# Kernel optimization log

Measured on AMD Instinct MI355X. Metric: run time of the kernel, lower is better.

The kernel has to match this reference:

```python
import jax, jax.numpy as jnp
import numpy as np

EMBED_DIM = 512
NUM_HEADS = 8
HEAD_DIM = EMBED_DIM // NUM_HEADS


def setup_inputs() -> dict:
    key = jax.random.key(0)
    ks = jax.random.split(key, 5)
    B, N, D = 2, 4096, EMBED_DIM
    s_in = 1.0 / np.sqrt(D)
    x = jax.random.normal(ks[0], (B, N, D), dtype=jnp.float32)
    qkv_w = jax.random.uniform(ks[1], (3 * D, D), dtype=jnp.float32, minval=-s_in, maxval=s_in)
    qkv_b = jax.random.uniform(ks[2], (3 * D,), dtype=jnp.float32, minval=-s_in, maxval=s_in)
    out_w = jax.random.uniform(ks[3], (D, D), dtype=jnp.float32, minval=-s_in, maxval=s_in)
    out_b = jax.random.uniform(ks[4], (D,), dtype=jnp.float32, minval=-s_in, maxval=s_in)
    return {"x": x, "qkv_w": qkv_w, "qkv_b": qkv_b, "out_w": out_w, "out_b": out_b}


def reference(x, qkv_w, qkv_b, out_w, out_b):
    B, N, D = x.shape
    H, Hd = NUM_HEADS, HEAD_DIM
    # qkv projection: [B,N,3D] -> [3,B,H,N,Hd]
    qkv = x @ qkv_w.T + qkv_b
    qkv = qkv.reshape(B, N, 3, H, Hd).transpose(2, 0, 3, 1, 4)
    q, k, v = qkv[0], qkv[1], qkv[2]
    scale = 1.0 / jnp.sqrt(jnp.asarray(Hd, dtype=x.dtype))
    scores = jnp.einsum("bhnd,bhmd->bhnm", q, k) * scale  # [B,H,N,N]
    weights = jax.nn.softmax(scores, axis=-1)
    out = jnp.einsum("bhnm,bhmd->bhnd", weights, v)  # [B,H,N,Hd]
    out = out.transpose(0, 2, 1, 3).reshape(B, N, D)
    return out @ out_w.T + out_b
```

## Files before the change

kernel.cpp:

```cpp
#include <hip/hip_runtime.h>

typedef __attribute__((ext_vector_type(8))) short short8;
typedef __attribute__((ext_vector_type(2))) float f32x2;
typedef __attribute__((ext_vector_type(4))) float f32x4;
typedef __attribute__((ext_vector_type(16))) float f32x16;
typedef unsigned short u16;
typedef unsigned int u32;

#define SCQ 0.18033688011112042f

__device__ __forceinline__ u16 f2b(float f) {
  unsigned u = __builtin_bit_cast(unsigned, f);
  u += 0x7FFFu + ((u >> 16) & 1u);
  return (u16)(u >> 16);
}

__device__ __forceinline__ u32 cvtpk(float a, float b) {
  u32 r;
  asm("v_cvt_pk_bf16_f32 %0, %1, %2" : "=v"(r) : "v"(a), "v"(b));
  return r;
}

__device__ __forceinline__ float ex2(float x) { return __builtin_amdgcn_exp2f(x); }

__global__ __launch_bounds__(256) void convert_k(
    const float* __restrict__ x, const float* __restrict__ w1, const float* __restrict__ w2,
    u16* __restrict__ xb, u16* __restrict__ w1b, u16* __restrict__ w2b) {
  const int NXv = (8192 * 512) / 4;
  const int NW1v = (1536 * 512) / 4;
  const int NW2v = (512 * 512) / 4;
  int i = blockIdx.x * 256 + threadIdx.x;
  const float4* src;
  u16* dst;
  int j;
  float scale = 1.0f;
  if (i < NXv) {
    src = (const float4*)x; dst = xb; j = i;
  } else if (i < NXv + NW1v) {
    j = i - NXv; src = (const float4*)w1; dst = w1b;
    if (j < (512 * 512) / 4) scale = SCQ;
  } else {
    j = i - NXv - NW1v;
    if (j >= NW2v) return;
    src = (const float4*)w2; dst = w2b;
  }
  float4 v = src[j];
  ushort4 o;
  o.x = f2b(v.x * scale); o.y = f2b(v.y * scale);
  o.z = f2b(v.z * scale); o.w = f2b(v.w * scale);
  *reinterpret_cast<ushort4*>(dst + (size_t)j * 4) = o;
}

__global__ __launch_bounds__(256) void qkv_gemm(
    const u16* __restrict__ Ab, const u16* __restrict__ Bw, const float* __restrict__ bias,
    u16* __restrict__ Qd, u16* __restrict__ Kd, u16* __restrict__ Vtd) {
  const int m0 = blockIdx.x * 128, n0 = blockIdx.y * 64;
  const int tid = threadIdx.x, wave = tid >> 6, lane = tid & 63;
  const int g = lane >> 4, lr = lane & 15;
  const int wm = (wave >> 1) * 64, wn = (wave & 1) * 32;
  __shared__ alignas(16) u16 Al[128][72];
  __shared__ alignas(16) u16 Bl[64][72];

  f32x4 acc[4][2];
#pragma unroll
  for (int mf = 0; mf < 4; ++mf)
#pragma unroll
    for (int nf = 0; nf < 2; ++nf)
#pragma unroll
      for (int r = 0; r < 4; ++r) acc[mf][nf][r] = 0.0f;

  const int rr = tid >> 3, cc = tid & 7;
  for (int k0 = 0; k0 < 512; k0 += 64) {
    __syncthreads();
#pragma unroll
    for (int it = 0; it < 4; ++it)
      *reinterpret_cast<short8*>(&Al[rr + it * 32][cc * 8]) =
          *reinterpret_cast<const short8*>(Ab + (size_t)(m0 + rr + it * 32) * 512 + k0 + cc * 8);
#pragma unroll
    for (int it = 0; it < 2; ++it)
      *reinterpret_cast<short8*>(&Bl[rr + it * 32][cc * 8]) =
          *reinterpret_cast<const short8*>(Bw + (size_t)(n0 + rr + it * 32) * 512 + k0 + cc * 8);
    __syncthreads();
#pragma unroll
    for (int kb = 0; kb < 2; ++kb) {
      short8 bf[2], af[4];
#pragma unroll
      for (int nf = 0; nf < 2; ++nf)
        bf[nf] = *reinterpret_cast<const short8*>(&Bl[wn + nf * 16 + lr][kb * 32 + g * 8]);
#pragma unroll
      for (int mf = 0; mf < 4; ++mf)
        af[mf] = *reinterpret_cast<const short8*>(&Al[wm + mf * 16 + lr][kb * 32 + g * 8]);
#pragma unroll
      for (int mf = 0; mf < 4; ++mf)
#pragma unroll
        for (int nf = 0; nf < 2; ++nf)
          acc[mf][nf] = __builtin_amdgcn_mfma_f32_16x16x32_bf16(af[mf], bf[nf], acc[mf][nf], 0, 0, 0);
    }
  }
#pragma unroll
  for (int mf = 0; mf < 4; ++mf)
#pragma unroll
    for (int nf = 0; nf < 2; ++nf)
#pragma unroll
      for (int r = 0; r < 4; ++r) {
        int row = m0 + wm + mf * 16 + g * 4 + r;
        int col = n0 + wn + nf * 16 + lr;
        float bv = bias[col];
        if (col < 512) bv *= SCQ;
        u16 val = f2b(acc[mf][nf][r] + bv);
        int which = col >> 9, dcol = col & 511;
        int h = dcol >> 6, hd = dcol & 63;
        int b = row >> 12, n = row & 4095;
        size_t hb = (size_t)(b * 8 + h);
        if (which == 0)      Qd[(hb * 4096 + n) * 64 + hd] = val;
        else if (which == 1) Kd[(hb * 4096 + n) * 64 + hd] = val;
        else                 Vtd[(hb * 64 + hd) * 4096 + n] = val;
      }
}

__global__ __launch_bounds__(256, 2) void attn10(
    const u16* __restrict__ Qd, const u16* __restrict__ Kd, const u16* __restrict__ Vtd,
    float* __restrict__ Op, float* __restrict__ Lp) {
  int f = blockIdx.x;
  int xcd = f & 7, slot = f >> 3;
  int bh = (xcd << 1) + (slot >> 6);
  int rem = slot & 63;
  int quarter = rem >> 4;
  int qb = rem & 15;

  const int tid = threadIdx.x, wave = tid >> 6, lane = tid & 63;
  const int hi = lane >> 5, lq = lane & 31;

  const u16* Qh = Qd + (size_t)bh * (4096 * 64);
  const u16* Kh = Kd + (size_t)bh * (4096 * 64);
  const u16* Vh = Vtd + (size_t)bh * (64 * 4096);
  float* Oh = Op + (size_t)quarter * (8192 * 512);
  float* Lh = Lp + (size_t)quarter * (16 * 4096);

  __shared__ alignas(16) u16 Kl[2][64 * 64];

  const int qrow_base = qb * 256 + wave * 64;

  short8 qf[2][4];
#pragma unroll
  for (int qt = 0; qt < 2; ++qt)
#pragma unroll
    for (int s = 0; s < 4; ++s)
      qf[qt][s] = *reinterpret_cast<const short8*>(
          Qh + (size_t)(qrow_base + qt * 32 + lq) * 64 + s * 16 + hi * 8);

  f32x16 acc[2][2];
#pragma unroll
  for (int qt = 0; qt < 2; ++qt)
#pragma unroll
    for (int dt = 0; dt < 2; ++dt)
#pragma unroll
      for (int i = 0; i < 16; ++i) acc[qt][dt][i] = 0.0f;

  f32x16 Z;
#pragma unroll
  for (int i = 0; i < 16; ++i) Z[i] = 0.0f;

  float lrun[2] = {0.0f, 0.0f};

  const int kv0 = quarter * 1024;
  const int g0 = tid, g1 = tid + 256;
  const int sr0 = g0 >> 3, sc0 = g0 & 7;
  const int sr1 = g1 >> 3, sc1 = g1 & 7;

  {
    short8 t0 = *reinterpret_cast<const short8*>(Kh + (size_t)(kv0 + sr0) * 64 + sc0 * 8);
    short8 t1 = *reinterpret_cast<const short8*>(Kh + (size_t)(kv0 + sr1) * 64 + sc1 * 8);
    *reinterpret_cast<short8*>(&Kl[0][sr0 * 64 + ((sc0 ^ (sr0 & 7)) << 3)]) = t0;
    *reinterpret_cast<short8*>(&Kl[0][sr1 * 64 + ((sc1 ^ (sr1 & 7)) << 3)]) = t1;
  }
  __syncthreads();

#pragma unroll 1
  for (int kt = 0; kt < 16; ++kt) {
    const int cur = kt & 1;
    const int kbase = kv0 + kt * 64;
    short8 t0, t1;
    const bool pf = (kt + 1 < 16);
    if (pf) {
      t0 = *reinterpret_cast<const short8*>(Kh + (size_t)(kbase + 64 + sr0) * 64 + sc0 * 8);
      t1 = *reinterpret_cast<const short8*>(Kh + (size_t)(kbase + 64 + sr1) * 64 + sc1 * 8);
    }

    f32x16 st[2][2];
#pragma unroll
    for (int s = 0; s < 4; ++s) {
      const int ch = ((2 * s + hi) ^ (lq & 7)) << 3;
      short8 kf0 = *reinterpret_cast<const short8*>(&Kl[cur][lq * 64 + ch]);
      short8 kf1 = *reinterpret_cast<const short8*>(&Kl[cur][(32 + lq) * 64 + ch]);
      if (s == 0) {
        st[0][0] = __builtin_amdgcn_mfma_f32_32x32x16_bf16(kf0, qf[0][0], Z, 0, 0, 0);
        st[0][1] = __builtin_amdgcn_mfma_f32_32x32x16_bf16(kf1, qf[0][0], Z, 0, 0, 0);
        st[1][0] = __builtin_amdgcn_mfma_f32_32x32x16_bf16(kf0, qf[1][0], Z, 0, 0, 0);
        st[1][1] = __builtin_amdgcn_mfma_f32_32x32x16_bf16(kf1, qf[1][0], Z, 0, 0, 0);
      } else {
        st[0][0] = __builtin_amdgcn_mfma_f32_32x32x16_bf16(kf0, qf[0][s], st[0][0], 0, 0, 0);
        st[0][1] = __builtin_amdgcn_mfma_f32_32x32x16_bf16(kf1, qf[0][s], st[0][1], 0, 0, 0);
        st[1][0] = __builtin_amdgcn_mfma_f32_32x32x16_bf16(kf0, qf[1][s], st[1][0], 0, 0, 0);
        st[1][1] = __builtin_amdgcn_mfma_f32_32x32x16_bf16(kf1, qf[1][s], st[1][1], 0, 0, 0);
      }
    }

    short8 vf[4][2];
#pragma unroll
    for (int ks = 0; ks < 4; ++ks)
#pragma unroll
      for (int dt = 0; dt < 2; ++dt)
        vf[ks][dt] = *reinterpret_cast<const short8*>(
            Vh + (size_t)(dt * 32 + lq) * 4096 + kbase + ks * 16 + hi * 8);

    short8 pb[2][4];
#pragma unroll
    for (int qt = 0; qt < 2; ++qt) {
      f32x2 p2[16];
#pragma unroll
      for (int j = 0; j < 8; ++j) {
        p2[j][0] = ex2(st[qt][0][2 * j]);
        p2[j][1] = ex2(st[qt][0][2 * j + 1]);
        p2[8 + j][0] = ex2(st[qt][1][2 * j]);
        p2[8 + j][1] = ex2(st[qt][1][2 * j + 1]);
      }
      f32x2 s0 = (p2[0] + p2[1]) + (p2[2] + p2[3]);
      f32x2 s1 = (p2[4] + p2[5]) + (p2[6] + p2[7]);
      f32x2 s2 = (p2[8] + p2[9]) + (p2[10] + p2[11]);
      f32x2 s3 = (p2[12] + p2[13]) + (p2[14] + p2[15]);
      f32x2 sm = (s0 + s1) + (s2 + s3);
      lrun[qt] += sm[0] + sm[1];
#pragma unroll
      for (int ks = 0; ks < 4; ++ks) {
        u32 wa = cvtpk(p2[4 * ks + 0][0], p2[4 * ks + 0][1]);
        u32 wb = cvtpk(p2[4 * ks + 2][0], p2[4 * ks + 2][1]);
        u32 wc = cvtpk(p2[4 * ks + 1][0], p2[4 * ks + 1][1]);
        u32 wd = cvtpk(p2[4 * ks + 3][0], p2[4 * ks + 3][1]);
        asm volatile("v_permlane32_swap_b32 %0, %1" : "+v"(wa), "+v"(wb));
        asm volatile("v_permlane32_swap_b32 %0, %1" : "+v"(wc), "+v"(wd));
        int4 wv;
        wv.x = (int)wa; wv.y = (int)wc; wv.z = (int)wb; wv.w = (int)wd;
        pb[qt][ks] = __builtin_bit_cast(short8, wv);
      }
    }

#pragma unroll
    for (int ks = 0; ks < 4; ++ks) {
      acc[0][0] = __builtin_amdgcn_mfma_f32_32x32x16_bf16(vf[ks][0], pb[0][ks], acc[0][0], 0, 0, 0);
      acc[0][1] = __builtin_amdgcn_mfma_f32_32x32x16_bf16(vf[ks][1], pb[0][ks], acc[0][1], 0, 0, 0);
      acc[1][0] = __builtin_amdgcn_mfma_f32_32x32x16_bf16(vf[ks][0], pb[1][ks], acc[1][0], 0, 0, 0);
      acc[1][1] = __builtin_amdgcn_mfma_f32_32x32x16_bf16(vf[ks][1], pb[1][ks], acc[1][1], 0, 0, 0);
    }

    if (pf) {
      *reinterpret_cast<short8*>(&Kl[cur ^ 1][sr0 * 64 + ((sc0 ^ (sr0 & 7)) << 3)]) = t0;
      *reinterpret_cast<short8*>(&Kl[cur ^ 1][sr1 * 64 + ((sc1 ^ (sr1 & 7)) << 3)]) = t1;
    }
    __syncthreads();
  }

  const int b = bh >> 3, h = bh & 7;
#pragma unroll
  for (int qt = 0; qt < 2; ++qt) {
    const int qn = qrow_base + qt * 32 + lq;
    const size_t rowoff = ((size_t)(b * 4096 + qn)) * 512 + h * 64;
#pragma unroll
    for (int dt = 0; dt < 2; ++dt)
#pragma unroll
      for (int t = 0; t < 4; ++t) {
        f32x4 v4;
        v4[0] = acc[qt][dt][4 * t + 0];
        v4[1] = acc[qt][dt][4 * t + 1];
        v4[2] = acc[qt][dt][4 * t + 2];
        v4[3] = acc[qt][dt][4 * t + 3];
        *reinterpret_cast<f32x4*>(Oh + rowoff + dt * 32 + t * 8 + hi * 4) = v4;
      }
    float lt = lrun[qt] + __shfl_xor(lrun[qt], 32);
    if (hi == 0) Lh[(bh << 12) + qn] = lt;
  }
}

__global__ __launch_bounds__(256) void combine_k(
    const float* __restrict__ Op, const float* __restrict__ Lp,
    u16* __restrict__ attnb) {
  int idx = blockIdx.x * 256 + threadIdx.x;
  int row = idx >> 7, c4 = idx & 127;
  int b = row >> 12, n = row & 4095, h = c4 >> 4;
  int li = (((b << 3) + h) << 12) + n;
  float l = (Lp[li] + Lp[li + 65536]) + (Lp[li + 131072] + Lp[li + 196608]);
  float inv = 1.0f / l;
  const int STRIDE = 8192 * 512 / 4;
  float4 o0 = reinterpret_cast<const float4*>(Op)[idx];
  float4 o1 = reinterpret_cast<const float4*>(Op)[idx + STRIDE];
  float4 o2 = reinterpret_cast<const float4*>(Op)[idx + 2 * STRIDE];
  float4 o3 = reinterpret_cast<const float4*>(Op)[idx + 3 * STRIDE];
  ushort4 o;
  o.x = f2b(((o0.x + o1.x) + (o2.x + o3.x)) * inv);
  o.y = f2b(((o0.y + o1.y) + (o2.y + o3.y)) * inv);
  o.z = f2b(((o0.z + o1.z) + (o2.z + o3.z)) * inv);
  o.w = f2b(((o0.w + o1.w) + (o2.w + o3.w)) * inv);
  *reinterpret_cast<ushort4*>(attnb + (size_t)idx * 4) = o;
}

__global__ __launch_bounds__(256) void out_gemm(
    const u16* __restrict__ Ab, const u16* __restrict__ Bw, const float* __restrict__ bias,
    float* __restrict__ out) {
  const int m0 = blockIdx.x * 128, n0 = blockIdx.y * 64;
  const int tid = threadIdx.x, wave = tid >> 6, lane = tid & 63;
  const int g = lane >> 4, lr = lane & 15;
  const int wm = (wave >> 1) * 64, wn = (wave & 1) * 32;
  __shared__ alignas(16) u16 Al[128][72];
  __shared__ alignas(16) u16 Bl[64][72];

  f32x4 acc[4][2];
#pragma unroll
  for (int mf = 0; mf < 4; ++mf)
#pragma unroll
    for (int nf = 0; nf < 2; ++nf)
#pragma unroll
      for (int r = 0; r < 4; ++r) acc[mf][nf][r] = 0.0f;

  const int rr = tid >> 3, cc = tid & 7;
  for (int k0 = 0; k0 < 512; k0 += 64) {
    __syncthreads();
#pragma unroll
    for (int it = 0; it < 4; ++it)
      *reinterpret_cast<short8*>(&Al[rr + it * 32][cc * 8]) =
          *reinterpret_cast<const short8*>(Ab + (size_t)(m0 + rr + it * 32) * 512 + k0 + cc * 8);
#pragma unroll
    for (int it = 0; it < 2; ++it)
      *reinterpret_cast<short8*>(&Bl[rr + it * 32][cc * 8]) =
          *reinterpret_cast<const short8*>(Bw + (size_t)(n0 + rr + it * 32) * 512 + k0 + cc * 8);
    __syncthreads();
#pragma unroll
    for (int kb = 0; kb < 2; ++kb) {
      short8 bf[2], af[4];
#pragma unroll
      for (int nf = 0; nf < 2; ++nf)
        bf[nf] = *reinterpret_cast<const short8*>(&Bl[wn + nf * 16 + lr][kb * 32 + g * 8]);
#pragma unroll
      for (int mf = 0; mf < 4; ++mf)
        af[mf] = *reinterpret_cast<const short8*>(&Al[wm + mf * 16 + lr][kb * 32 + g * 8]);
#pragma unroll
      for (int mf = 0; mf < 4; ++mf)
#pragma unroll
        for (int nf = 0; nf < 2; ++nf)
          acc[mf][nf] = __builtin_amdgcn_mfma_f32_16x16x32_bf16(af[mf], bf[nf], acc[mf][nf], 0, 0, 0);
    }
  }
#pragma unroll
  for (int mf = 0; mf < 4; ++mf)
#pragma unroll
    for (int nf = 0; nf < 2; ++nf)
#pragma unroll
      for (int r = 0; r < 4; ++r) {
        int row = m0 + wm + mf * 16 + g * 4 + r;
        int col = n0 + wn + nf * 16 + lr;
        out[(size_t)row * 512 + col] = acc[mf][nf][r] + bias[col];
      }
}

extern "C" void kernel_launch(void* const* d_in, const int* in_sizes, int n_in,
                              void* d_out, int out_size, void* d_ws, size_t ws_size,
                              hipStream_t stream) {
  const float* x = (const float*)d_in[0];
  const float* qkv_w = (const float*)d_in[1];
  const float* qkv_b = (const float*)d_in[2];
  const float* out_w = (const float*)d_in[3];
  const float* out_b = (const float*)d_in[4];
  float* out = (float*)d_out;

  char* ws = (char*)d_ws;
  u16* xb    = (u16*)(ws + 0);
  u16* w1b   = (u16*)(ws + 8388608);
  u16* w2b   = (u16*)(ws + 9961472);
  u16* Qd    = (u16*)(ws + 10485760);
  u16* Kd    = (u16*)(ws + 18874368);
  u16* Vtd   = (u16*)(ws + 27262976);
  u16* attnb = (u16*)(ws + 35651584);
  float* Op  = (float*)(ws + 44040192);
  float* Lp  = (float*)(ws + 111149056);

  convert_k<<<5120, 256, 0, stream>>>(x, qkv_w, out_w, xb, w1b, w2b);
  qkv_gemm<<<dim3(64, 24), 256, 0, stream>>>(xb, w1b, qkv_b, Qd, Kd, Vtd);
  attn10<<<1024, 256, 0, stream>>>(Qd, Kd, Vtd, Op, Lp);
  combine_k<<<4096, 256, 0, stream>>>(Op, Lp, attnb);
  out_gemm<<<dim3(64, 8), 256, 0, stream>>>(attnb, w2b, out_b, out);
}
```

Before: 146.9 us.

## Drop split-KV combine, use direct-to-LDS loads and larger QKV GEMM tiles

The attention kernel no longer splits the KV range into quarters. Each 2-wave block now walks all 4096 keys and writes normalized bf16 output directly, so the fp32 partial buffers and the combine kernel are removed. K tiles and the QKV GEMM operands are loaded with global_load_lds into XOR-swizzled LDS, and the QKV GEMM N tile grows from 64 to 128. This cuts large fp32 partial traffic and one launch, but the attention grid drops to 512 blocks of 128 threads with a longer serial loop, which may reduce occupancy and latency hiding.

```diff
diff --git a/kernel.cpp b/kernel.cpp
--- a/kernel.cpp
+++ b/kernel.cpp
@@ -22,6 +22,12 @@
 }
 
 __device__ __forceinline__ float ex2(float x) { return __builtin_amdgcn_exp2f(x); }
+
+__device__ __forceinline__ void gl_lds16(const u16* g, u16* l) {
+  __builtin_amdgcn_global_load_lds(
+      (const __attribute__((address_space(1))) unsigned int*)g,
+      (__attribute__((address_space(3))) unsigned int*)l, 16, 0, 0);
+}
 
 __global__ __launch_bounds__(256) void convert_k(
     const float* __restrict__ x, const float* __restrict__ w1, const float* __restrict__ w2,
@@ -54,53 +60,56 @@
 __global__ __launch_bounds__(256) void qkv_gemm(
     const u16* __restrict__ Ab, const u16* __restrict__ Bw, const float* __restrict__ bias,
     u16* __restrict__ Qd, u16* __restrict__ Kd, u16* __restrict__ Vtd) {
-  const int m0 = blockIdx.x * 128, n0 = blockIdx.y * 64;
+  const int m0 = blockIdx.x * 128, n0 = blockIdx.y * 128;
   const int tid = threadIdx.x, wave = tid >> 6, lane = tid & 63;
   const int g = lane >> 4, lr = lane & 15;
-  const int wm = (wave >> 1) * 64, wn = (wave & 1) * 32;
-  __shared__ alignas(16) u16 Al[128][72];
-  __shared__ alignas(16) u16 Bl[64][72];
-
-  f32x4 acc[4][2];
+  const int wm = (wave >> 1) * 64, wn = (wave & 1) * 64;
+  __shared__ alignas(16) u16 Al[128 * 64];
+  __shared__ alignas(16) u16 Bl[128 * 64];
+
+  f32x4 acc[4][4];
 #pragma unroll
   for (int mf = 0; mf < 4; ++mf)
 #pragma unroll
-    for (int nf = 0; nf < 2; ++nf)
+    for (int nf = 0; nf < 4; ++nf)
 #pragma unroll
       for (int r = 0; r < 4; ++r) acc[mf][nf][r] = 0.0f;
 
-  const int rr = tid >> 3, cc = tid & 7;
+  const int gid0 = wave * 64 + lane;
+
   for (int k0 = 0; k0 < 512; k0 += 64) {
     __syncthreads();
 #pragma unroll
-    for (int it = 0; it < 4; ++it)
-      *reinterpret_cast<short8*>(&Al[rr + it * 32][cc * 8]) =
-          *reinterpret_cast<const short8*>(Ab + (size_t)(m0 + rr + it * 32) * 512 + k0 + cc * 8);
-#pragma unroll
-    for (int it = 0; it < 2; ++it)
-      *reinterpret_cast<short8*>(&Bl[rr + it * 32][cc * 8]) =
-          *reinterpret_cast<const short8*>(Bw + (size_t)(n0 + rr + it * 32) * 512 + k0 + cc * 8);
+    for (int c = 0; c < 4; ++c) {
+      const int gid = c * 256 + gid0;
+      const int row = gid >> 3;
+      const int col = ((gid & 7) ^ (row & 7)) << 3;
+      gl_lds16(Ab + (size_t)(m0 + row) * 512 + k0 + col, Al + (size_t)(c * 256 + wave * 64) * 8);
+      gl_lds16(Bw + (size_t)(n0 + row) * 512 + k0 + col, Bl + (size_t)(c * 256 + wave * 64) * 8);
+    }
     __syncthreads();
 #pragma unroll
     for (int kb = 0; kb < 2; ++kb) {
-      short8 bf[2], af[4];
-#pragma unroll
-      for (int nf = 0; nf < 2; ++nf)
-        bf[nf] = *reinterpret_cast<const short8*>(&Bl[wn + nf * 16 + lr][kb * 32 + g * 8]);
+      short8 bf[4], af[4];
+#pragma unroll
+      for (int nf = 0; nf < 4; ++nf)
+        bf[nf] = *reinterpret_cast<const short8*>(
+            Bl + (wn + nf * 16 + lr) * 64 + (((kb * 4 + g) ^ (lr & 7)) << 3));
 #pragma unroll
       for (int mf = 0; mf < 4; ++mf)
-        af[mf] = *reinterpret_cast<const short8*>(&Al[wm + mf * 16 + lr][kb * 32 + g * 8]);
+        af[mf] = *reinterpret_cast<const short8*>(
+            Al + (wm + mf * 16 + lr) * 64 + (((kb * 4 + g) ^ (lr & 7)) << 3));
 #pragma unroll
       for (int mf = 0; mf < 4; ++mf)
 #pragma unroll
-        for (int nf = 0; nf < 2; ++nf)
+        for (int nf = 0; nf < 4; ++nf)
           acc[mf][nf] = __builtin_amdgcn_mfma_f32_16x16x32_bf16(af[mf], bf[nf], acc[mf][nf], 0, 0, 0);
     }
   }
 #pragma unroll
   for (int mf = 0; mf < 4; ++mf)
 #pragma unroll
-    for (int nf = 0; nf < 2; ++nf)
+    for (int nf = 0; nf < 4; ++nf)
 #pragma unroll
       for (int r = 0; r < 4; ++r) {
         int row = m0 + wm + mf * 16 + g * 4 + r;
@@ -118,15 +127,13 @@
       }
 }
 
-__global__ __launch_bounds__(256, 2) void attn10(
+__global__ __launch_bounds__(128, 2) void attn11(
     const u16* __restrict__ Qd, const u16* __restrict__ Kd, const u16* __restrict__ Vtd,
-    float* __restrict__ Op, float* __restrict__ Lp) {
+    u16* __restrict__ attnb) {
   int f = blockIdx.x;
   int xcd = f & 7, slot = f >> 3;
-  int bh = (xcd << 1) + (slot >> 6);
-  int rem = slot & 63;
-  int quarter = rem >> 4;
-  int qb = rem & 15;
+  int bh = (xcd << 1) + (slot >> 5);
+  int qb = slot & 31;
 
   const int tid = threadIdx.x, wave = tid >> 6, lane = tid & 63;
   const int hi = lane >> 5, lq = lane & 31;
@@ -134,12 +141,10 @@
   const u16* Qh = Qd + (size_t)bh * (4096 * 64);
   const u16* Kh = Kd + (size_t)bh * (4096 * 64);
   const u16* Vh = Vtd + (size_t)bh * (64 * 4096);
-  float* Oh = Op + (size_t)quarter * (8192 * 512);
-  float* Lh = Lp + (size_t)quarter * (16 * 4096);
 
   __shared__ alignas(16) u16 Kl[2][64 * 64];
 
-  const int qrow_base = qb * 256 + wave * 64;
+  const int qrow_base = qb * 128 + wave * 64;
 
   short8 qf[2][4];
 #pragma unroll
@@ -163,28 +168,31 @@
 
   float lrun[2] = {0.0f, 0.0f};
 
-  const int kv0 = quarter * 1024;
-  const int g0 = tid, g1 = tid + 256;
-  const int sr0 = g0 >> 3, sc0 = g0 & 7;
-  const int sr1 = g1 >> 3, sc1 = g1 & 7;
-
-  {
-    short8 t0 = *reinterpret_cast<const short8*>(Kh + (size_t)(kv0 + sr0) * 64 + sc0 * 8);
-    short8 t1 = *reinterpret_cast<const short8*>(Kh + (size_t)(kv0 + sr1) * 64 + sc1 * 8);
-    *reinterpret_cast<short8*>(&Kl[0][sr0 * 64 + ((sc0 ^ (sr0 & 7)) << 3)]) = t0;
-    *reinterpret_cast<short8*>(&Kl[0][sr1 * 64 + ((sc1 ^ (sr1 & 7)) << 3)]) = t1;
+  const int gid0 = wave * 64 + lane;
+
+#pragma unroll
+  for (int c = 0; c < 4; ++c) {
+    const int gid = c * 128 + gid0;
+    const int row = gid >> 3;
+    const int col = ((gid & 7) ^ (row & 7)) << 3;
+    gl_lds16(Kh + (size_t)row * 64 + col, &Kl[0][(c * 128 + wave * 64) * 8]);
   }
   __syncthreads();
 
 #pragma unroll 1
-  for (int kt = 0; kt < 16; ++kt) {
+  for (int kt = 0; kt < 64; ++kt) {
     const int cur = kt & 1;
-    const int kbase = kv0 + kt * 64;
-    short8 t0, t1;
-    const bool pf = (kt + 1 < 16);
-    if (pf) {
-      t0 = *reinterpret_cast<const short8*>(Kh + (size_t)(kbase + 64 + sr0) * 64 + sc0 * 8);
-      t1 = *reinterpret_cast<const short8*>(Kh + (size_t)(kbase + 64 + sr1) * 64 + sc1 * 8);
+    const int kbase = kt * 64;
+
+    if (kt + 1 < 64) {
+      const u16* kn = Kh + (size_t)(kbase + 64) * 64;
+#pragma unroll
+      for (int c = 0; c < 4; ++c) {
+        const int gid = c * 128 + gid0;
+        const int row = gid >> 3;
+        const int col = ((gid & 7) ^ (row & 7)) << 3;
+        gl_lds16(kn + (size_t)row * 64 + col, &Kl[cur ^ 1][(c * 128 + wave * 64) * 8]);
+      }
     }
 
     f32x16 st[2][2];
@@ -253,54 +261,28 @@
       acc[1][1] = __builtin_amdgcn_mfma_f32_32x32x16_bf16(vf[ks][1], pb[1][ks], acc[1][1], 0, 0, 0);
     }
 
-    if (pf) {
-      *reinterpret_cast<short8*>(&Kl[cur ^ 1][sr0 * 64 + ((sc0 ^ (sr0 & 7)) << 3)]) = t0;
-      *reinterpret_cast<short8*>(&Kl[cur ^ 1][sr1 * 64 + ((sc1 ^ (sr1 & 7)) << 3)]) = t1;
-    }
     __syncthreads();
   }
 
   const int b = bh >> 3, h = bh & 7;
 #pragma unroll
   for (int qt = 0; qt < 2; ++qt) {
+    float lt = lrun[qt] + __shfl_xor(lrun[qt], 32);
+    const float inv = 1.0f / lt;
     const int qn = qrow_base + qt * 32 + lq;
-    const size_t rowoff = ((size_t)(b * 4096 + qn)) * 512 + h * 64;
+    u16* dst = attnb + (size_t)(b * 4096 + qn) * 512 + h * 64;
 #pragma unroll
     for (int dt = 0; dt < 2; ++dt)
 #pragma unroll
       for (int t = 0; t < 4; ++t) {
-        f32x4 v4;
-        v4[0] = acc[qt][dt][4 * t + 0];
-        v4[1] = acc[qt][dt][4 * t + 1];
-        v4[2] = acc[qt][dt][4 * t + 2];
-        v4[3] = acc[qt][dt][4 * t + 3];
-        *reinterpret_cast<f32x4*>(Oh + rowoff + dt * 32 + t * 8 + hi * 4) = v4;
-      }
-    float lt = lrun[qt] + __shfl_xor(lrun[qt], 32);
-    if (hi == 0) Lh[(bh << 12) + qn] = lt;
-  }
-}
-
-__global__ __launch_bounds__(256) void combine_k(
-    const float* __restrict__ Op, const float* __restrict__ Lp,
-    u16* __restrict__ attnb) {
-  int idx = blockIdx.x * 256 + threadIdx.x;
-  int row = idx >> 7, c4 = idx & 127;
-  int b = row >> 12, n = row & 4095, h = c4 >> 4;
-  int li = (((b << 3) + h) << 12) + n;
-  float l = (Lp[li] + Lp[li + 65536]) + (Lp[li + 131072] + Lp[li + 196608]);
-  float inv = 1.0f / l;
-  const int STRIDE = 8192 * 512 / 4;
-  float4 o0 = reinterpret_cast<const float4*>(Op)[idx];
-  float4 o1 = reinterpret_cast<const float4*>(Op)[idx + STRIDE];
-  float4 o2 = reinterpret_cast<const float4*>(Op)[idx + 2 * STRIDE];
-  float4 o3 = reinterpret_cast<const float4*>(Op)[idx + 3 * STRIDE];
-  ushort4 o;
-  o.x = f2b(((o0.x + o1.x) + (o2.x + o3.x)) * inv);
-  o.y = f2b(((o0.y + o1.y) + (o2.y + o3.y)) * inv);
-  o.z = f2b(((o0.z + o1.z) + (o2.z + o3.z)) * inv);
-  o.w = f2b(((o0.w + o1.w) + (o2.w + o3.w)) * inv);
-  *reinterpret_cast<ushort4*>(attnb + (size_t)idx * 4) = o;
+        ushort4 o;
+        o.x = f2b(acc[qt][dt][4 * t + 0] * inv);
+        o.y = f2b(acc[qt][dt][4 * t + 1] * inv);
+        o.z = f2b(acc[qt][dt][4 * t + 2] * inv);
+        o.w = f2b(acc[qt][dt][4 * t + 3] * inv);
+        *reinterpret_cast<ushort4*>(dst + dt * 32 + t * 8 + hi * 4) = o;
+      }
+  }
 }
 
 __global__ __launch_bounds__(256) void out_gemm(
@@ -379,12 +361,9 @@
   u16* Kd    = (u16*)(ws + 18874368);
   u16* Vtd   = (u16*)(ws + 27262976);
   u16* attnb = (u16*)(ws + 35651584);
-  float* Op  = (float*)(ws + 44040192);
-  float* Lp  = (float*)(ws + 111149056);
 
   convert_k<<<5120, 256, 0, stream>>>(x, qkv_w, out_w, xb, w1b, w2b);
-  qkv_gemm<<<dim3(64, 24), 256, 0, stream>>>(xb, w1b, qkv_b, Qd, Kd, Vtd);
-  attn10<<<1024, 256, 0, stream>>>(Qd, Kd, Vtd, Op, Lp);
-  combine_k<<<4096, 256, 0, stream>>>(Op, Lp, attnb);
+  qkv_gemm<<<dim3(64, 12), 256, 0, stream>>>(xb, w1b, qkv_b, Qd, Kd, Vtd);
+  attn11<<<512, 128, 0, stream>>>(Qd, Kd, Vtd, attnb);
   out_gemm<<<dim3(64, 8), 256, 0, stream>>>(attnb, w2b, out_b, out);
 }
```

After: 166.3 us. 1.13x slower.
